# Performance work log

Measured on AMD Instinct MI355X. Metric: run time of the kernel, lower is better.

## Reference

```python
import jax, jax.numpy as jnp
import numpy as np

MARGIN_M = 0.5   # ArcFace additive angular margin
SCALE_S = 64.0   # ArcFace logit scale


def _l2norm(x, axis=-1, eps=1e-12):
    return x / jnp.sqrt(jnp.sum(x * x, axis=axis, keepdims=True) + eps)


def _arcface_ce(logits, labels):
    """Apply ArcFace margin at target column, scale, softmax-CE. logits [B,C], labels [B]."""
    B = logits.shape[0]
    rows = jnp.arange(B)
    t = logits[rows, labels]                          # target cosine, [B]
    tc = jnp.clip(t, -1.0 + 1e-7, 1.0 - 1e-7)
    cos_m, sin_m = np.cos(MARGIN_M), np.sin(MARGIN_M)
    # cos(theta + m); hard-margin fallback: t - sin(pi-m)*m when t <= cos(pi-m)
    marg = tc * cos_m - jnp.sqrt(1.0 - tc * tc) * sin_m
    thresh = np.cos(np.pi - MARGIN_M)
    mm = np.sin(np.pi - MARGIN_M) * MARGIN_M
    final_t = jnp.where(t > thresh, marg, t - mm)
    logits_m = logits.at[rows, labels].set(final_t) * SCALE_S   # [B, C]
    logp = jax.nn.log_softmax(logits_m, axis=1)
    return -jnp.mean(logp[rows, labels])


def setup_inputs() -> dict:
    key = jax.random.key(0)
    k1, k2, k3 = jax.random.split(key, 3)
    B, D, C, RD = 256, 512, 100000, 8
    return {
        "local_embeddings": jax.random.normal(k1, (B, D), dtype=jnp.float32),
        "weight": jax.random.normal(k2, (C, D), dtype=jnp.float32) * 0.01,
        "local_labels": jax.random.randint(k3, (B, RD), 0, C, dtype=jnp.int64),
        "random_diff": RD,
    }


def reference(local_embeddings, weight, local_labels, random_diff):
    B = local_embeddings.shape[0]
    # no_grad label-column shuffle: keep 3 random columns out of random_diff
    noise = jax.random.uniform(jax.random.key(42), (B, random_diff))
    ids_keep = jnp.argsort(noise, axis=1)[:, :3]                       # [B, 3]
    labels3 = jnp.take_along_axis(local_labels, ids_keep, axis=1)      # [B, 3]
    # world_size=1, sample_rate=1: all labels are positive local indices
    norm_emb = _l2norm(local_embeddings)                               # [B, D]
    norm_w = _l2norm(weight)                                           # [C, D]
    logits = jnp.clip(norm_emb @ norm_w.T, -1.0, 1.0)                  # [B, C]
    loss = (_arcface_ce(logits, labels3[:, 0])
            + _arcface_ce(logits, labels3[:, 1])
            + _arcface_ce(logits, labels3[:, 2])) / 3.0
    return loss
```

## Files before the change

### kernel.cpp

```cpp
#include <hip/hip_runtime.h>
#include <hip/hip_bf16.h>
#include <stdint.h>

#define K_D 512
#define N_C 100000
#define SCALE 64.0f

#define COS_M 0.87758256189037271612f
#define SIN_M 0.47942553860420300027f
#define TH   (-0.87758256189037271612f)
#define MM_C  0.23971276930210150013f

typedef __attribute__((ext_vector_type(8))) short bf16x8;
typedef __attribute__((ext_vector_type(4))) float f32x4;

#define GZ_BLOCKS 1250
#define CHUNKS_PB 5
#define ZSTRIDE 1280

#define OFF_INVNE 0
#define OFF_EMB   1024
#define OFF_TP    263168
#define OFF_ZROW  269312
#define OFF_ZPART 270336

__device__ __forceinline__ ushort f2bf(float f) {
    __hip_bfloat16 h = __float2bfloat16(f);
    return __builtin_bit_cast(ushort, h);
}

__device__ __forceinline__ void async16(const float* src, float* dst) {
    __builtin_amdgcn_global_load_lds(
        (const __attribute__((address_space(1))) void*)src,
        (__attribute__((address_space(3))) void*)dst,
        16, 0, 0);
}

__global__ __launch_bounds__(256) void prep_emb(const float* __restrict__ E,
                                                ushort* __restrict__ Ebf,
                                                float* __restrict__ invne) {
    int w = threadIdx.x >> 6, lane = threadIdx.x & 63;
    int row = blockIdx.x * 4 + w;
    const float4* src = (const float4*)(E + (size_t)row * K_D);
    float4 a = src[2 * lane];
    float4 b = src[2 * lane + 1];
    float ss = a.x*a.x + a.y*a.y + a.z*a.z + a.w*a.w
             + b.x*b.x + b.y*b.y + b.z*b.z + b.w*b.w;
    #pragma unroll
    for (int m = 32; m >= 1; m >>= 1) ss += __shfl_xor(ss, m, 64);
    uint4 pk;
    pk.x = (uint32_t)f2bf(a.x) | ((uint32_t)f2bf(a.y) << 16);
    pk.y = (uint32_t)f2bf(a.z) | ((uint32_t)f2bf(a.w) << 16);
    pk.z = (uint32_t)f2bf(b.x) | ((uint32_t)f2bf(b.y) << 16);
    pk.w = (uint32_t)f2bf(b.z) | ((uint32_t)f2bf(b.w) << 16);
    const int kstep = lane >> 2, gg = lane & 3;
    const size_t slot = ((size_t)(row >> 4) * 16 + kstep) * 64 + (row & 15) + (gg << 4);
    ((uint4*)Ebf)[slot] = pk;
    if (lane == 0) invne[row] = rsqrtf(ss + 1e-12f);
}

__device__ __forceinline__ void threefry(uint32_t x0, uint32_t x1, uint32_t& o0, uint32_t& o1) {
    const uint32_t k0 = 0u, k1 = 42u;
    const uint32_t k2 = k0 ^ k1 ^ 0x1BD11BDAu;
    const uint32_t ks[3] = {k0, k1, k2};
    x0 += k0; x1 += k1;
    const int rot0[4] = {13, 15, 26, 6};
    const int rot1[4] = {17, 29, 16, 24};
    #pragma unroll
    for (int grp = 0; grp < 5; ++grp) {
        const int* r = (grp & 1) ? rot1 : rot0;
        #pragma unroll
        for (int i = 0; i < 4; ++i) {
            x0 += x1;
            x1 = (x1 << r[i]) | (x1 >> (32 - r[i]));
            x1 ^= x0;
        }
        x0 += ks[(grp + 1) % 3];
        x1 += ks[(grp + 2) % 3] + (uint32_t)(grp + 1);
    }
    o0 = x0; o1 = x1;
}

__global__ __launch_bounds__(256) void target_kernel(const float* __restrict__ E,
                                                     const float* __restrict__ W,
                                                     const int* __restrict__ ll,
                                                     float* __restrict__ tp) {
    int w = threadIdx.x >> 6, lane = threadIdx.x & 63;
    int p = blockIdx.x * 4 + w;
    int b = p / 3;
    int jj = p - b * 3;
    float u[8];
    #pragma unroll
    for (int j = 0; j < 8; ++j) {
        int n = b * 8 + j;
        uint32_t x0, x1, o0, o1;
        if (n < 1024) { x0 = (uint32_t)n; x1 = (uint32_t)(n + 1024); }
        else          { x0 = (uint32_t)(n - 1024); x1 = (uint32_t)n; }
        threefry(x0, x1, o0, o1);
        uint32_t bits = (n < 1024) ? o0 : o1;
        uint32_t fb = (bits >> 9) | 0x3F800000u;
        u[j] = __builtin_bit_cast(float, fb) - 1.0f;
    }
    bool used[8] = {false,false,false,false,false,false,false,false};
    int sel = 0;
    for (int s = 0; s <= jj; ++s) {
        float bv = 2.0f; int bi = 0;
        for (int i = 0; i < 8; ++i)
            if (!used[i] && u[i] < bv) { bv = u[i]; bi = i; }
        used[bi] = true;
        sel = bi;
    }
    int c = ll[b * 8 + sel];

    const float4* ep = (const float4*)(E + (size_t)b * K_D);
    const float4* wp = (const float4*)(W + (size_t)c * K_D);
    float4 e0 = ep[lane], e1 = ep[lane + 64];
    float4 w0 = wp[lane], w1 = wp[lane + 64];
    float dot = e0.x*w0.x + e0.y*w0.y + e0.z*w0.z + e0.w*w0.w
              + e1.x*w1.x + e1.y*w1.y + e1.z*w1.z + e1.w*w1.w;
    float esq = e0.x*e0.x + e0.y*e0.y + e0.z*e0.z + e0.w*e0.w
              + e1.x*e1.x + e1.y*e1.y + e1.z*e1.z + e1.w*e1.w;
    float wsq = w0.x*w0.x + w0.y*w0.y + w0.z*w0.z + w0.w*w0.w
              + w1.x*w1.x + w1.y*w1.y + w1.z*w1.z + w1.w*w1.w;
    #pragma unroll
    for (int m = 32; m >= 1; m >>= 1) {
        dot += __shfl_xor(dot, m, 64);
        esq += __shfl_xor(esq, m, 64);
        wsq += __shfl_xor(wsq, m, 64);
    }
    if (lane == 0) {
        float t = dot * rsqrtf(esq + 1e-12f) * rsqrtf(wsq + 1e-12f);
        t = fminf(1.0f, fmaxf(-1.0f, t));
        float tc = fminf(1.0f - 1e-7f, fmaxf(-1.0f + 1e-7f, t));
        float marg = tc * COS_M - sqrtf(fmaxf(0.0f, 1.0f - tc * tc)) * SIN_M;
        float ft = (t > TH) ? marg : (t - MM_C);
        tp[p * 2]     = t;
        tp[p * 2 + 1] = ft;
    }
}

__global__ __launch_bounds__(512, 4) void gemm_z(const float* __restrict__ W,
                                                 const ushort* __restrict__ Ebf,
                                                 const float* __restrict__ invne,
                                                 float* __restrict__ zpart) {
    __shared__ float Bbuf[2][16 * 512];
    __shared__ float ine_lds[256];

    const int tid  = threadIdx.x;
    const int lane = tid & 63, wv = tid >> 6;
    const int r16  = lane & 15, g = lane >> 4;
    const int s    = r16 & 7;
    const int bx   = blockIdx.x;
    const int cbase = bx * (16 * CHUNKS_PB);

    if (tid < 256) ine_lds[tid] = invne[tid];

    #define STAGE(ch, b)                                                          \
        {                                                                         \
            _Pragma("unroll")                                                     \
            for (int rr = 0; rr < 2; ++rr) {                                      \
                const int r = wv * 2 + rr;                                        \
                const float* src = W + (size_t)(cbase + (ch) * 16 + r) * K_D;     \
                _Pragma("unroll")                                                 \
                for (int hb = 0; hb < 2; ++hb) {                                  \
                    const int hp = hb * 64 + lane;                                \
                    async16(src + ((hp ^ (r & 7)) << 2),                          \
                            &Bbuf[b][r * 512 + hb * 256]);                        \
                }                                                                 \
            }                                                                     \
        }

    STAGE(0, 0);
    __syncthreads();

    float zacc[2][4] = {};

    for (int ch = 0; ch < CHUNKS_PB; ++ch) {
        const int cur = ch & 1;
        if (ch + 1 < CHUNKS_PB) STAGE(ch + 1, cur ^ 1);

        f32x4 acc0 = {}, acc1 = {};
        float ssq = 0.f;
        const float4* bp = (const float4*)&Bbuf[cur][r16 * 512];
        const ushort* ap0 = Ebf + ((size_t)(wv * 2 + 0) * 16) * 64 * 8 + lane * 8;
        const ushort* ap1 = Ebf + ((size_t)(wv * 2 + 1) * 16) * 64 * 8 + lane * 8;

        #pragma unroll 4
        for (int ks = 0; ks < 16; ++ks) {
            bf16x8 a0 = *(const bf16x8*)(ap0 + (size_t)ks * 512);
            bf16x8 a1 = *(const bf16x8*)(ap1 + (size_t)ks * 512);
            const int h = ks * 8 + g * 2;
            float4 f0 = bp[(h)     ^ s];
            float4 f1 = bp[(h + 1) ^ s];
            ssq += f0.x*f0.x + f0.y*f0.y + f0.z*f0.z + f0.w*f0.w
                 + f1.x*f1.x + f1.y*f1.y + f1.z*f1.z + f1.w*f1.w;
            bf16x8 bv;
            bv[0] = (short)f2bf(f0.x); bv[1] = (short)f2bf(f0.y);
            bv[2] = (short)f2bf(f0.z); bv[3] = (short)f2bf(f0.w);
            bv[4] = (short)f2bf(f1.x); bv[5] = (short)f2bf(f1.y);
            bv[6] = (short)f2bf(f1.z); bv[7] = (short)f2bf(f1.w);
            acc0 = __builtin_amdgcn_mfma_f32_16x16x32_bf16(a0, bv, acc0, 0, 0, 0);
            acc1 = __builtin_amdgcn_mfma_f32_16x16x32_bf16(a1, bv, acc1, 0, 0, 0);
        }

        float sr = ssq;
        sr += __shfl_xor(sr, 16, 64);
        sr += __shfl_xor(sr, 32, 64);
        const float inw = rsqrtf(sr + 1e-12f);

        #pragma unroll
        for (int i = 0; i < 4; ++i) {
            const int row0 = (wv * 2 + 0) * 16 + g * 4 + i;
            const int row1 = (wv * 2 + 1) * 16 + g * 4 + i;
            float c0 = acc0[i] * inw * ine_lds[row0];
            float c1 = acc1[i] * inw * ine_lds[row1];
            c0 = fminf(1.0f, fmaxf(-1.0f, c0));
            c1 = fminf(1.0f, fmaxf(-1.0f, c1));
            zacc[0][i] += __expf(SCALE * c0 - 64.0f);
            zacc[1][i] += __expf(SCALE * c1 - 64.0f);
        }
        __syncthreads();
    }

    #pragma unroll
    for (int mi = 0; mi < 2; ++mi)
        #pragma unroll
        for (int i = 0; i < 4; ++i) {
            float v = zacc[mi][i];
            v += __shfl_xor(v, 1, 64);
            v += __shfl_xor(v, 2, 64);
            v += __shfl_xor(v, 4, 64);
            v += __shfl_xor(v, 8, 64);
            if (r16 == 0) {
                const int row = (wv * 2 + mi) * 16 + g * 4 + i;
                zpart[(size_t)row * ZSTRIDE + bx] = v;
            }
        }
}

__global__ __launch_bounds__(256) void zrow_kernel(const float* __restrict__ zpart,
                                                   float* __restrict__ zrow) {
    const int b = blockIdx.x;
    float sum = 0.f;
    for (int t = threadIdx.x; t < GZ_BLOCKS; t += 256)
        sum += zpart[(size_t)b * ZSTRIDE + t];
    __shared__ float red[256];
    red[threadIdx.x] = sum;
    __syncthreads();
    for (int st = 128; st >= 1; st >>= 1) {
        if (threadIdx.x < st) red[threadIdx.x] += red[threadIdx.x + st];
        __syncthreads();
    }
    if (threadIdx.x == 0) zrow[b] = red[0];
}

__global__ __launch_bounds__(256) void loss_kernel(const float* __restrict__ zrow,
                                                   const float* __restrict__ tp,
                                                   float* __restrict__ out) {
    const int b = threadIdx.x;
    const float Z = zrow[b];
    float lsum = 0.f;
    #pragma unroll
    for (int j = 0; j < 3; ++j) {
        float t  = tp[(b * 3 + j) * 2];
        float ft = tp[(b * 3 + j) * 2 + 1];
        float S = Z - expf(SCALE * t - 64.0f) + expf(SCALE * ft - 64.0f);
        lsum += logf(S) + 64.0f - SCALE * ft;
    }
    __shared__ float red[256];
    red[b] = lsum;
    __syncthreads();
    for (int st = 128; st >= 1; st >>= 1) {
        if (b < st) red[b] += red[b + st];
        __syncthreads();
    }
    if (b == 0) out[0] = red[0] / 768.0f;
}

extern "C" void kernel_launch(void* const* d_in, const int* in_sizes, int n_in,
                              void* d_out, int out_size, void* d_ws, size_t ws_size,
                              hipStream_t stream) {
    const float* E = (const float*)d_in[0];
    const float* W = (const float*)d_in[1];
    const int*  LL = (const int*)d_in[2];
    char* ws = (char*)d_ws;
    float*  invne = (float*)(ws + OFF_INVNE);
    ushort* Ebf   = (ushort*)(ws + OFF_EMB);
    float*  tp    = (float*)(ws + OFF_TP);
    float*  zrow  = (float*)(ws + OFF_ZROW);
    float*  zpart = (float*)(ws + OFF_ZPART);
    float*  out   = (float*)d_out;

    hipLaunchKernelGGL(prep_emb,      dim3(64),        dim3(256), 0, stream, E, Ebf, invne);
    hipLaunchKernelGGL(target_kernel, dim3(192),       dim3(256), 0, stream, E, W, LL, tp);
    hipLaunchKernelGGL(gemm_z,        dim3(GZ_BLOCKS), dim3(512), 0, stream, W, Ebf, invne, zpart);
    hipLaunchKernelGGL(zrow_kernel,   dim3(256),       dim3(256), 0, stream, zpart, zrow);
    hipLaunchKernelGGL(loss_kernel,   dim3(1),         dim3(256), 0, stream, zrow, tp, out);
}
```

Measured before the change: 100.5 us.

## Pad LDS rows and use explicit vmcnt waits for the W double-buffer pipeline

Replaces the XOR-swizzled LDS layout for W tiles with rows padded to 516 floats, so each lane reads contiguous float4 values without index XOR. It also swaps __syncthreads for explicit s_waitcnt vmcnt counts plus raw s_barrier, so the next chunk's async loads can stay in flight while the current chunk is computed. The Ebf pointer setup is hoisted out of the loop. The hand-counted vmcnt and the dropped waits around the ine_lds writes and the Ebf global loads risk races or stalls. The padding also adds a little LDS use.

```diff
diff --git a/kernel.cpp b/kernel.cpp
--- a/kernel.cpp
+++ b/kernel.cpp
@@ -17,6 +17,7 @@
 #define GZ_BLOCKS 1250
 #define CHUNKS_PB 5
 #define ZSTRIDE 1280
+#define ROWF 516
 
 #define OFF_INVNE 0
 #define OFF_EMB   1024
@@ -29,7 +30,7 @@
     return __builtin_bit_cast(ushort, h);
 }
 
-__device__ __forceinline__ void async16(const float* src, float* dst) {
+__device__ __forceinline__ void async16(const void* src, void* dst) {
     __builtin_amdgcn_global_load_lds(
         (const __attribute__((address_space(1))) void*)src,
         (__attribute__((address_space(3))) void*)dst,
@@ -143,55 +144,57 @@
                                                  const ushort* __restrict__ Ebf,
                                                  const float* __restrict__ invne,
                                                  float* __restrict__ zpart) {
-    __shared__ float Bbuf[2][16 * 512];
+    __shared__ float Wb[2][16 * ROWF];
     __shared__ float ine_lds[256];
 
     const int tid  = threadIdx.x;
     const int lane = tid & 63, wv = tid >> 6;
     const int r16  = lane & 15, g = lane >> 4;
-    const int s    = r16 & 7;
     const int bx   = blockIdx.x;
     const int cbase = bx * (16 * CHUNKS_PB);
 
     if (tid < 256) ine_lds[tid] = invne[tid];
 
-    #define STAGE(ch, b)                                                          \
-        {                                                                         \
-            _Pragma("unroll")                                                     \
-            for (int rr = 0; rr < 2; ++rr) {                                      \
-                const int r = wv * 2 + rr;                                        \
-                const float* src = W + (size_t)(cbase + (ch) * 16 + r) * K_D;     \
-                _Pragma("unroll")                                                 \
-                for (int hb = 0; hb < 2; ++hb) {                                  \
-                    const int hp = hb * 64 + lane;                                \
-                    async16(src + ((hp ^ (r & 7)) << 2),                          \
-                            &Bbuf[b][r * 512 + hb * 256]);                        \
-                }                                                                 \
-            }                                                                     \
+    #define STAGE(ch, b)                                                        \
+        {                                                                       \
+            _Pragma("unroll")                                                   \
+            for (int rr = 0; rr < 2; ++rr) {                                    \
+                const int r = wv * 2 + rr;                                      \
+                const float* src = W + (size_t)(cbase + (ch) * 16 + r) * K_D    \
+                                     + lane * 4;                                \
+                async16(src,        &Wb[b][r * ROWF]);                          \
+                async16(src + 256,  &Wb[b][r * ROWF + 256]);                    \
+            }                                                                   \
         }
 
     STAGE(0, 0);
-    __syncthreads();
+
+    const ushort* ap0 = Ebf + ((size_t)(wv * 2 + 0) * 16) * 64 * 8 + lane * 8;
+    const ushort* ap1 = Ebf + ((size_t)(wv * 2 + 1) * 16) * 64 * 8 + lane * 8;
 
     float zacc[2][4] = {};
 
     for (int ch = 0; ch < CHUNKS_PB; ++ch) {
         const int cur = ch & 1;
-        if (ch + 1 < CHUNKS_PB) STAGE(ch + 1, cur ^ 1);
+        if (ch + 1 < CHUNKS_PB) {
+            STAGE(ch + 1, cur ^ 1);
+            asm volatile("s_waitcnt vmcnt(4)" ::: "memory");
+        } else {
+            asm volatile("s_waitcnt vmcnt(0)" ::: "memory");
+        }
+        __builtin_amdgcn_s_barrier();
+        __builtin_amdgcn_sched_barrier(0);
 
         f32x4 acc0 = {}, acc1 = {};
         float ssq = 0.f;
-        const float4* bp = (const float4*)&Bbuf[cur][r16 * 512];
-        const ushort* ap0 = Ebf + ((size_t)(wv * 2 + 0) * 16) * 64 * 8 + lane * 8;
-        const ushort* ap1 = Ebf + ((size_t)(wv * 2 + 1) * 16) * 64 * 8 + lane * 8;
+        const float4* bp = (const float4*)&Wb[cur][r16 * ROWF];
 
         #pragma unroll 4
         for (int ks = 0; ks < 16; ++ks) {
             bf16x8 a0 = *(const bf16x8*)(ap0 + (size_t)ks * 512);
             bf16x8 a1 = *(const bf16x8*)(ap1 + (size_t)ks * 512);
-            const int h = ks * 8 + g * 2;
-            float4 f0 = bp[(h)     ^ s];
-            float4 f1 = bp[(h + 1) ^ s];
+            float4 f0 = bp[ks * 8 + g * 2];
+            float4 f1 = bp[ks * 8 + g * 2 + 1];
             ssq += f0.x*f0.x + f0.y*f0.y + f0.z*f0.z + f0.w*f0.w
                  + f1.x*f1.x + f1.y*f1.y + f1.z*f1.z + f1.w*f1.w;
             bf16x8 bv;
@@ -219,7 +222,7 @@
             zacc[0][i] += __expf(SCALE * c0 - 64.0f);
             zacc[1][i] += __expf(SCALE * c1 - 64.0f);
         }
-        __syncthreads();
+        __builtin_amdgcn_s_barrier();
     }
 
     #pragma unroll
```

Measured after the change: 99.13 us. About the same (-1.3%).
